# Performance work log

Hardware: AMD Instinct MI355X
Metric: run time of the kernel (lower is better)

## Reference

```python
import jax, jax.numpy as jnp
import numpy as np

EMBED = 512
NHEAD = 16
HDIM = EMBED // NHEAD
HIDDEN = 512  # Mlp hidden is hard-coded to 512
EPS_LN = 1e-6
EPS_ATT = 1e-6


def layernorm(x, gamma, beta):
    mu = jnp.mean(x, axis=-1, keepdims=True)
    var = jnp.mean(jnp.square(x - mu), axis=-1, keepdims=True)
    return (x - mu) * jax.lax.rsqrt(var + EPS_LN) * gamma + beta


def setup_inputs() -> dict:
    key = jax.random.key(0)
    ks = jax.random.split(key, 16)
    B, N, C = 8, 4096, EMBED
    s = 1.0 / np.sqrt(C)
    inp = {
        "x": jax.random.normal(ks[0], (B, N, C), dtype=jnp.float32),
        # projection weights stored as (in, out); torch Linear uses x @ W.T
        "Wq": jax.random.normal(ks[1], (C, C), dtype=jnp.float32) * s,
        "Wk": jax.random.normal(ks[2], (C, C), dtype=jnp.float32) * s,
        "Wv": jax.random.normal(ks[3], (C, C), dtype=jnp.float32) * s,
        "Wm": jax.random.normal(ks[4], (C, C), dtype=jnp.float32) * s,
        "W1": jax.random.normal(ks[5], (C, HIDDEN), dtype=jnp.float32) * s,
        "b1": jax.random.normal(ks[6], (HIDDEN,), dtype=jnp.float32) * 1e-6,
        "W2": jax.random.normal(ks[7], (HIDDEN, C), dtype=jnp.float32) * (1.0 / np.sqrt(HIDDEN)),
        "b2": jax.random.normal(ks[8], (C,), dtype=jnp.float32) * 1e-6,
        "g_att": jnp.ones((C,), dtype=jnp.float32),
        "b_att": jnp.zeros((C,), dtype=jnp.float32),
        "g_ffn": jnp.ones((C,), dtype=jnp.float32),
        "b_ffn": jnp.zeros((C,), dtype=jnp.float32),
    }
    return inp


def reference(x, Wq, Wk, Wv, Wm, W1, b1, W2, b2, g_att, b_att, g_ffn, b_ffn):
    B, N, C = x.shape
    # --- attention sub-block ---
    h = layernorm(x, g_att, b_att)
    q = (h @ Wq).reshape(B, N, NHEAD, HDIM)
    k = (h @ Wk).reshape(B, N, NHEAD, HDIM)
    v = (h @ Wv).reshape(B, N, NHEAD, HDIM)
    Q = jax.nn.elu(q) + 1.0  # feature map: elu(x)+1
    K = jax.nn.elu(k) + 1.0
    v = v / N
    KV = jnp.einsum('nshd,nshv->nhdv', K, v)
    Z = 1.0 / (jnp.einsum('nlhd,nhd->nlh', Q, K.sum(axis=1)) + EPS_ATT)
    msg = jnp.einsum('nlhd,nhdv->nlhv', Q, KV) * Z[..., None] * N
    msg = msg.reshape(B, N, C) @ Wm
    x = x + msg
    # --- feed-forward sub-block ---
    h2 = layernorm(x, g_ffn, b_ffn)
    f = jax.nn.gelu(h2 @ W1 + b1, approximate=False) @ W2 + b2
    return x + f
```

## Files before the change

kernel.cpp:

```cpp
#include <hip/hip_runtime.h>
#include <hip/hip_bf16.h>
#include <math.h>

typedef unsigned short u16;
typedef __attribute__((ext_vector_type(8))) __bf16 bf16x8;
typedef __attribute__((ext_vector_type(4))) float floatx4;

#define SEQ   4096
#define BATCH 8
#define ROWS  32768
#define C     512
#define NH    16
#define HD    32

__device__ inline u16 f2bf(float f) {
    union { float f; unsigned u; } v; v.f = f;
    unsigned r = (v.u + 0x7FFFu + ((v.u >> 16) & 1u)) >> 16;
    return (u16)r;
}
__device__ inline float bf2f(u16 h) {
    union { unsigned u; float f; } v; v.u = ((unsigned)h) << 16;
    return v.f;
}

__device__ inline void g2lds16(const u16* g, u16* l) {
    __builtin_amdgcn_global_load_lds((const __attribute__((address_space(1))) unsigned*)g,
                                     (__attribute__((address_space(3))) unsigned*)l, 16, 0, 0);
}

__global__ __launch_bounds__(256) void prep_weights(
    const float* __restrict__ Wq, const float* __restrict__ Wk,
    const float* __restrict__ Wv, const float* __restrict__ Wm,
    const float* __restrict__ W1, const float* __restrict__ W2,
    u16* __restrict__ Wqkvt, u16* __restrict__ Wmt,
    u16* __restrict__ W1t, u16* __restrict__ W2t)
{
    int blk = blockIdx.x;
    int mat = blk >> 6;
    int tile = blk & 63;
    int k0 = (tile >> 3) * 64, n0 = (tile & 7) * 64;
    const float* src; u16* dst;
    switch (mat) {
        case 0: src = Wq; dst = Wqkvt;              break;
        case 1: src = Wk; dst = Wqkvt + 512*512;    break;
        case 2: src = Wv; dst = Wqkvt + 2*512*512;  break;
        case 3: src = Wm; dst = Wmt;                break;
        case 4: src = W1; dst = W1t;                break;
        default: src = W2; dst = W2t;               break;
    }
    __shared__ float ts[64][65];
    int t = threadIdx.x;
    #pragma unroll
    for (int i = 0; i < 16; i++) {
        int e = i * 256 + t;
        int kr = e >> 6, nc = e & 63;
        ts[kr][nc] = src[(size_t)(k0 + kr) * 512 + n0 + nc];
    }
    __syncthreads();
    #pragma unroll
    for (int i = 0; i < 2; i++) {
        int e = i * 256 + t;
        int nr = e >> 3, kc0 = (e & 7) * 8;
        union { uint4 v; u16 u[8]; } o;
        #pragma unroll
        for (int q = 0; q < 8; q++) o.u[q] = f2bf(ts[kc0 + q][nr]);
        *(uint4*)(dst + (size_t)(n0 + nr) * 512 + k0 + kc0) = o.v;
    }
}

__global__ __launch_bounds__(256) void ln_kernel(
    const float* __restrict__ in, const float* __restrict__ g,
    const float* __restrict__ b, u16* __restrict__ out)
{
    int row  = blockIdx.x * 4 + (threadIdx.x >> 6);
    int lane = threadIdx.x & 63;
    const float* p = in + (size_t)row * C + lane * 8;
    float4 v0 = *(const float4*)p;
    float4 v1 = *(const float4*)(p + 4);
    float s  = v0.x + v0.y + v0.z + v0.w + v1.x + v1.y + v1.z + v1.w;
    float s2 = v0.x*v0.x + v0.y*v0.y + v0.z*v0.z + v0.w*v0.w
             + v1.x*v1.x + v1.y*v1.y + v1.z*v1.z + v1.w*v1.w;
    #pragma unroll
    for (int off = 1; off < 64; off <<= 1) {
        s  += __shfl_xor(s, off);
        s2 += __shfl_xor(s2, off);
    }
    float mean = s * (1.f / C);
    float var  = s2 * (1.f / C) - mean * mean;
    float inv  = rsqrtf(var + 1e-6f);
    int c = lane * 8;
    float4 g0 = *(const float4*)(g + c), g1 = *(const float4*)(g + c + 4);
    float4 b0 = *(const float4*)(b + c), b1 = *(const float4*)(b + c + 4);
    union { uint4 v; u16 u[8]; } o;
    o.u[0] = f2bf((v0.x - mean) * inv * g0.x + b0.x);
    o.u[1] = f2bf((v0.y - mean) * inv * g0.y + b0.y);
    o.u[2] = f2bf((v0.z - mean) * inv * g0.z + b0.z);
    o.u[3] = f2bf((v0.w - mean) * inv * g0.w + b0.w);
    o.u[4] = f2bf((v1.x - mean) * inv * g1.x + b1.x);
    o.u[5] = f2bf((v1.y - mean) * inv * g1.y + b1.y);
    o.u[6] = f2bf((v1.z - mean) * inv * g1.z + b1.z);
    o.u[7] = f2bf((v1.w - mean) * inv * g1.w + b1.w);
    *(uint4*)(out + (size_t)row * C + c) = o.v;
}

template <int EPI>
__global__ __launch_bounds__(256, 2) void gemm_tile(
    const u16* __restrict__ A, const u16* __restrict__ Bt,
    int K, int ldc, int nx, int ypx,
    u16* __restrict__ outb, float* __restrict__ outf,
    const float* __restrict__ bias, const float* __restrict__ resid)
{
    __shared__ u16 lsA[128 * 64];
    __shared__ u16 lsB[128 * 64];
    const int t = threadIdx.x;
    const int w = t >> 6, l = t & 63, lr = l & 15, quad = l >> 4;
    const int g = blockIdx.x;
    const int xcd = g & 7;
    const int q = g >> 3;
    const int npg = nx * 2;
    const int grp = q / npg, rem = q - grp * npg;
    const int tx = rem >> 1;
    const int ty = xcd * ypx + grp * 2 + (rem & 1);
    const int m0 = ty * 128, n0 = tx * 128;
    const int RW = (w >> 1) * 64, CW = (w & 1) * 64;

    floatx4 acc[4][4];
    #pragma unroll
    for (int i = 0; i < 4; i++)
        #pragma unroll
        for (int j = 0; j < 4; j++) { floatx4 z = {0.f, 0.f, 0.f, 0.f}; acc[i][j] = z; }

    const int srow = w * 32 + (l >> 3);
    const int scol = (((l & 7) - (l >> 3)) & 7) * 8;
    const u16* Ag = A  + (size_t)(m0 + srow) * K + scol;
    const u16* Bg = Bt + (size_t)(n0 + srow) * K + scol;
    u16* lAw = lsA + w * 2048;
    u16* lBw = lsB + w * 2048;

    for (int kk = 0; kk < K; kk += 64) {
        __syncthreads();
        #pragma unroll
        for (int c = 0; c < 4; c++) {
            g2lds16(Ag + (size_t)(c * 8) * K + kk, lAw + c * 512);
            g2lds16(Bg + (size_t)(c * 8) * K + kk, lBw + c * 512);
        }
        __syncthreads();
        #pragma unroll
        for (int ks = 0; ks < 2; ks++) {
            bf16x8 af[4], bfr[4];
            const int m = ((ks * 4 + quad + (lr & 7)) & 7) * 8;
            #pragma unroll
            for (int i = 0; i < 4; i++) {
                af[i]  = *(const bf16x8*)(lsA + (RW + i * 16 + lr) * 64 + m);
                bfr[i] = *(const bf16x8*)(lsB + (CW + i * 16 + lr) * 64 + m);
            }
            #pragma unroll
            for (int i = 0; i < 4; i++)
                #pragma unroll
                for (int j = 0; j < 4; j++)
                    acc[i][j] = __builtin_amdgcn_mfma_f32_16x16x32_bf16(af[i], bfr[j], acc[i][j], 0, 0, 0);
        }
    }

    #pragma unroll
    for (int i = 0; i < 4; i++) {
        #pragma unroll
        for (int j = 0; j < 4; j++) {
            #pragma unroll
            for (int r = 0; r < 4; r++) {
                int row = m0 + RW + i * 16 + quad * 4 + r;
                int col = n0 + CW + j * 16 + lr;
                float v = acc[i][j][r];
                size_t idx = (size_t)row * ldc + col;
                if constexpr (EPI == 0) {
                    if (col < 1024) v = v > 0.f ? v + 1.f : __expf(v);
                    else            v *= (1.0f / SEQ);
                    outb[idx] = f2bf(v);
                } else if constexpr (EPI == 1) {
                    outf[idx] = resid[idx] + v;
                } else if constexpr (EPI == 2) {
                    v += bias[col];
                    v = 0.5f * v * (1.f + erff(v * 0.70710678118f));
                    outb[idx] = f2bf(v);
                } else {
                    outf[idx] = outf[idx] + v + bias[col];
                }
            }
        }
    }
}

__global__ __launch_bounds__(256) void kv_reduce(
    const u16* __restrict__ qkv, float* __restrict__ Pkv, float* __restrict__ PKsum)
{
    const int bh = blockIdx.x;
    const int b = bh >> 4, h = bh & 15;
    const int chunk = blockIdx.y;
    const int t = threadIdx.x;
    const int w = t >> 6, l = t & 63, lr = l & 15, quad = l >> 4;
    __shared__ u16 lds[4 * 2 * 2048];

    const int sbase = chunk * 512 + w * 128;
    const u16* qbase = qkv + (size_t)b * SEQ * 1536 + 512 + h * HD;

    const int sl0 = l >> 2;
    const int sl1 = 16 + sl0;
    const int cl  = l & 3;
    const int cg0 = (cl + (sl0 >> 3)) & 3;
    const int cg1 = (cl + (sl1 >> 3)) & 3;
    const int gof0 = sl0 * 1536 + cg0 * 8;
    const int gof1 = sl1 * 1536 + cg1 * 8;

    u16* myl = lds + w * 4096;

    const int offA0 = quad * 256 + ((((lr >> 3) + 0) - quad) & 3) * 8 + (lr & 7);
    const int offA1 = quad * 256 + ((((lr >> 3) + 2) - quad) & 3) * 8 + (lr & 7);

    floatx4 a00 = {0,0,0,0}, a01 = {0,0,0,0}, a10 = {0,0,0,0}, a11 = {0,0,0,0};
    float ks0 = 0.f, ks1 = 0.f;

    {
        const u16* gK = qbase + (size_t)sbase * 1536;
        g2lds16(gK + gof0,       myl);
        g2lds16(gK + gof1,       myl + 512);
        g2lds16(gK + 512 + gof0, myl + 1024);
        g2lds16(gK + 512 + gof1, myl + 1536);
    }
    #pragma unroll
    for (int st = 0; st < 4; st++) {
        if (st < 3) {
            const u16* gK = qbase + (size_t)(sbase + (st + 1) * 32) * 1536;
            u16* nl = myl + ((st + 1) & 1) * 2048;
            g2lds16(gK + gof0,       nl);
            g2lds16(gK + gof1,       nl + 512);
            g2lds16(gK + 512 + gof0, nl + 1024);
            g2lds16(gK + 512 + gof1, nl + 1536);
        }
        __syncthreads();
        const u16* lK = myl + (st & 1) * 2048;
        const u16* lV = lK + 1024;
        union { bf16x8 v; u16 u[8]; } fa0, fa1, fb0, fb1;
        #pragma unroll
        for (int j = 0; j < 8; j++) {
            fa0.u[j] = lK[offA0 + j * 32];
            fa1.u[j] = lK[offA1 + j * 32];
            fb0.u[j] = lV[offA0 + j * 32];
            fb1.u[j] = lV[offA1 + j * 32];
        }
        #pragma unroll
        for (int j = 0; j < 8; j++) { ks0 += bf2f(fa0.u[j]); ks1 += bf2f(fa1.u[j]); }
        a00 = __builtin_amdgcn_mfma_f32_16x16x32_bf16(fa0.v, fb0.v, a00, 0, 0, 0);
        a01 = __builtin_amdgcn_mfma_f32_16x16x32_bf16(fa0.v, fb1.v, a01, 0, 0, 0);
        a10 = __builtin_amdgcn_mfma_f32_16x16x32_bf16(fa1.v, fb0.v, a10, 0, 0, 0);
        a11 = __builtin_amdgcn_mfma_f32_16x16x32_bf16(fa1.v, fb1.v, a11, 0, 0, 0);
    }

    const int p = bh * 32 + chunk * 4 + w;
    float* dst = Pkv + (size_t)p * 1024;
    floatx4 accs[2][2] = {{a00, a01}, {a10, a11}};
    #pragma unroll
    for (int i = 0; i < 2; i++)
        #pragma unroll
        for (int j = 0; j < 2; j++)
            #pragma unroll
            for (int r = 0; r < 4; r++)
                dst[(i * 16 + quad * 4 + r) * 32 + j * 16 + lr] = accs[i][j][r];

    float k0 = ks0 + __shfl_xor(ks0, 16); k0 += __shfl_xor(k0, 32);
    float k1 = ks1 + __shfl_xor(ks1, 16); k1 += __shfl_xor(k1, 32);
    if (quad == 0) {
        PKsum[p * 32 + lr]      = k0;
        PKsum[p * 32 + 16 + lr] = k1;
    }
}

__global__ __launch_bounds__(256) void kv_final(
    const float* __restrict__ Pkv, const float* __restrict__ PKsum,
    float* __restrict__ KV, float* __restrict__ Ksum)
{
    const int blk = blockIdx.x;
    const int bh = blk >> 2, part = blk & 3;
    const int t = threadIdx.x;
    const float* src = Pkv + (size_t)bh * 32 * 1024 + part * 256 + t;
    float a = 0.f;
    #pragma unroll 4
    for (int p = 0; p < 32; p++) a += src[(size_t)p * 1024];
    KV[(size_t)bh * 1024 + part * 256 + t] = a;
    if (part == 0 && t < 32) {
        float s = 0.f;
        for (int p = 0; p < 32; p++) s += PKsum[(bh * 32 + p) * 32 + t];
        Ksum[bh * 32 + t] = s;
    }
}

__global__ __launch_bounds__(256) void msg_kernel(
    const u16* __restrict__ qkv, const float* __restrict__ KV,
    const float* __restrict__ Ksum, u16* __restrict__ msg)
{
    int blk = blockIdx.x;
    int b = blk >> 7;
    int r0 = (blk & 127) * 32;
    int t = threadIdx.x;
    int h = t >> 4;
    int vd = (t & 15) * 2;
    float kv0[32], kv1[32], ksr[32];
    const float* kvh = KV + ((size_t)b * 16 + h) * 1024;
    const float* ksh = Ksum + (b * 16 + h) * 32;
    #pragma unroll
    for (int d = 0; d < 32; d++) {
        kv0[d] = kvh[d * 32 + vd];
        kv1[d] = kvh[d * 32 + vd + 1];
        ksr[d] = ksh[d];
    }
    __shared__ u16 Qs[4 * 512];
    const int srr = t >> 6;
    const int scc = (t & 63) * 8;
    for (int rg = 0; rg < 32; rg += 4) {
        size_t row = (size_t)b * SEQ + r0 + rg;
        uint4 qv = *(const uint4*)(qkv + (row + srr) * 1536 + scc);
        __syncthreads();
        *(uint4*)(Qs + srr * 512 + scc) = qv;
        __syncthreads();
        #pragma unroll
        for (int r2 = 0; r2 < 4; r2++) {
            const u16* qp = Qs + r2 * 512 + h * HD;
            float q[32];
            #pragma unroll
            for (int i0 = 0; i0 < 32; i0 += 8) {
                union { uint4 v; u16 u[8]; } uu;
                uu.v = *(const uint4*)(qp + i0);
                #pragma unroll
                for (int jq = 0; jq < 8; jq++) q[i0 + jq] = bf2f(uu.u[jq]);
            }
            float zdot = 0.f, m0 = 0.f, m1 = 0.f;
            #pragma unroll
            for (int d = 0; d < 32; d++) {
                float qd = q[d];
                zdot += qd * ksr[d];
                m0   += qd * kv0[d];
                m1   += qd * kv1[d];
            }
            float z = (float)SEQ / (zdot + 1e-6f);
            unsigned pack = (unsigned)f2bf(m0 * z) | ((unsigned)f2bf(m1 * z) << 16);
            *(unsigned*)(msg + (row + r2) * C + h * HD + vd) = pack;
        }
    }
}

extern "C" void kernel_launch(void* const* d_in, const int* in_sizes, int n_in,
                              void* d_out, int out_size, void* d_ws, size_t ws_size,
                              hipStream_t stream) {
    const float* x     = (const float*)d_in[0];
    const float* Wq    = (const float*)d_in[1];
    const float* Wk    = (const float*)d_in[2];
    const float* Wv    = (const float*)d_in[3];
    const float* Wm    = (const float*)d_in[4];
    const float* W1    = (const float*)d_in[5];
    const float* b1    = (const float*)d_in[6];
    const float* W2    = (const float*)d_in[7];
    const float* b2    = (const float*)d_in[8];
    const float* g_att = (const float*)d_in[9];
    const float* b_att = (const float*)d_in[10];
    const float* g_ffn = (const float*)d_in[11];
    const float* b_ffn = (const float*)d_in[12];
    float* out = (float*)d_out;

    char* ws = (char*)d_ws;
    u16*   Wqkvt = (u16*)(ws);
    u16*   Wmt   = (u16*)(ws + 0x180000);
    u16*   W1t   = (u16*)(ws + 0x200000);
    u16*   W2t   = (u16*)(ws + 0x280000);
    float* KV    = (float*)(ws + 0x300000);
    float* Ksum  = (float*)(ws + 0x380000);
    u16*   hb    = (u16*)(ws + 0x400000);
    float* Pkv   = (float*)(ws + 0x400000);
    float* PKsum = (float*)(ws + 0x1400000);
    u16*   qkv   = (u16*)(ws + 0x2400000);
    u16*   h2    = qkv;
    u16*   f1    = (u16*)(ws + 0x4400000);

    prep_weights<<<6 * 64, 256, 0, stream>>>(Wq, Wk, Wv, Wm, W1, W2,
                                             Wqkvt, Wmt, W1t, W2t);
    ln_kernel<<<ROWS / 4, 256, 0, stream>>>(x, g_att, b_att, hb);
    gemm_tile<0><<<3072, 256, 0, stream>>>(hb, Wqkvt, 512, 1536, 12, 32,
                                           qkv, nullptr, nullptr, nullptr);
    kv_reduce<<<dim3(128, 8), 256, 0, stream>>>(qkv, Pkv, PKsum);
    kv_final<<<512, 256, 0, stream>>>(Pkv, PKsum, KV, Ksum);
    msg_kernel<<<1024, 256, 0, stream>>>(qkv, KV, Ksum, hb);
    gemm_tile<1><<<1024, 256, 0, stream>>>(hb, Wmt, 512, 512, 4, 32,
                                           nullptr, out, nullptr, x);
    ln_kernel<<<ROWS / 4, 256, 0, stream>>>(out, g_ffn, b_ffn, h2);
    gemm_tile<2><<<1024, 256, 0, stream>>>(h2, W1t, 512, 512, 4, 32,
                                           f1, nullptr, b1, nullptr);
    gemm_tile<3><<<1024, 256, 0, stream>>>(f1, W2t, 512, 512, 4, 32,
                                           nullptr, out, b2, nullptr);
}
```

Before: 383.1 us.

## Fuse Wm projection GEMM with residual add and FFN layernorm

Adds a GEMM kernel whose blocks cover full 512-column rows (64 rows by 512 cols per block), so the residual add and the second layernorm can run in the epilogue. Row statistics are reduced across lanes and waves through shared memory. This removes the separate ln_kernel launch and its re-read of the fp32 residual output. The cost is a large LDS footprint (about 72KB), fewer blocks (512) and a different tile shape, which may lower occupancy. Variance is computed as E[x^2]-mean^2, which is less numerically stable.

Measured after the change: 432.4 us. 12.9% more time.

```diff
diff --git a/kernel.cpp b/kernel.cpp
--- a/kernel.cpp
+++ b/kernel.cpp
@@ -190,6 +190,134 @@
     }
 }
 
+__global__ __launch_bounds__(512, 4) void gemm_wmln(
+    const u16* __restrict__ A, const u16* __restrict__ Bt,
+    const float* __restrict__ resid, const float* __restrict__ gf,
+    const float* __restrict__ bf, float* __restrict__ out,
+    u16* __restrict__ h2)
+{
+    __shared__ u16 lsA[64 * 64];
+    __shared__ u16 lsB[512 * 64];
+    __shared__ float ps[64][4][2];
+    __shared__ float stats[64][2];
+
+    const int t = threadIdx.x;
+    const int w = t >> 6, l = t & 63, lr = l & 15, quad = l >> 4;
+    const int wr = w >> 2, wc = w & 3;
+    const int m0 = blockIdx.x * 64;
+
+    const int srow = l >> 3;
+    const int scol = (((l & 7) - srow) & 7) * 8;
+    const u16* Ag = A  + (size_t)(m0 + w * 8 + srow) * 512 + scol;
+    const u16* Bg = Bt + (size_t)(w * 64 + srow) * 512 + scol;
+    u16* lAw = lsA + w * 512;
+    u16* lBw = lsB + w * 4096;
+
+    floatx4 acc[2][8];
+    #pragma unroll
+    for (int i = 0; i < 2; i++)
+        #pragma unroll
+        for (int j = 0; j < 8; j++) { floatx4 z = {0.f, 0.f, 0.f, 0.f}; acc[i][j] = z; }
+
+    for (int kk = 0; kk < 512; kk += 64) {
+        __syncthreads();
+        g2lds16(Ag + kk, lAw);
+        #pragma unroll
+        for (int c = 0; c < 8; c++)
+            g2lds16(Bg + (size_t)(c * 8) * 512 + kk, lBw + c * 512);
+        __syncthreads();
+        #pragma unroll
+        for (int ks = 0; ks < 2; ks++) {
+            bf16x8 af[2], bfr[8];
+            const int m = ((ks * 4 + quad + (lr & 7)) & 7) * 8;
+            af[0] = *(const bf16x8*)(lsA + (wr * 32 + lr) * 64 + m);
+            af[1] = *(const bf16x8*)(lsA + (wr * 32 + 16 + lr) * 64 + m);
+            #pragma unroll
+            for (int j = 0; j < 8; j++)
+                bfr[j] = *(const bf16x8*)(lsB + (wc * 128 + j * 16 + lr) * 64 + m);
+            #pragma unroll
+            for (int i = 0; i < 2; i++)
+                #pragma unroll
+                for (int j = 0; j < 8; j++)
+                    acc[i][j] = __builtin_amdgcn_mfma_f32_16x16x32_bf16(af[i], bfr[j], acc[i][j], 0, 0, 0);
+        }
+    }
+
+    float s[2][4], s2[2][4];
+    #pragma unroll
+    for (int i = 0; i < 2; i++)
+        #pragma unroll
+        for (int r = 0; r < 4; r++) { s[i][r] = 0.f; s2[i][r] = 0.f; }
+    #pragma unroll
+    for (int i = 0; i < 2; i++) {
+        #pragma unroll
+        for (int j = 0; j < 8; j++) {
+            #pragma unroll
+            for (int r = 0; r < 4; r++) {
+                int row = m0 + wr * 32 + i * 16 + quad * 4 + r;
+                int col = wc * 128 + j * 16 + lr;
+                size_t idx = (size_t)row * 512 + col;
+                float x2 = resid[idx] + acc[i][j][r];
+                out[idx] = x2;
+                acc[i][j][r] = x2;
+                s[i][r]  += x2;
+                s2[i][r] += x2 * x2;
+            }
+        }
+    }
+    #pragma unroll
+    for (int i = 0; i < 2; i++)
+        #pragma unroll
+        for (int r = 0; r < 4; r++) {
+            #pragma unroll
+            for (int off = 1; off < 16; off <<= 1) {
+                s[i][r]  += __shfl_xor(s[i][r], off);
+                s2[i][r] += __shfl_xor(s2[i][r], off);
+            }
+        }
+    if (lr == 0) {
+        #pragma unroll
+        for (int i = 0; i < 2; i++)
+            #pragma unroll
+            for (int r = 0; r < 4; r++) {
+                int rl = wr * 32 + i * 16 + quad * 4 + r;
+                ps[rl][wc][0] = s[i][r];
+                ps[rl][wc][1] = s2[i][r];
+            }
+    }
+    __syncthreads();
+    if (t < 64) {
+        float ssum = ps[t][0][0] + ps[t][1][0] + ps[t][2][0] + ps[t][3][0];
+        float ssq  = ps[t][0][1] + ps[t][1][1] + ps[t][2][1] + ps[t][3][1];
+        float mean = ssum * (1.f / C);
+        float var  = ssq * (1.f / C) - mean * mean;
+        stats[t][0] = mean;
+        stats[t][1] = rsqrtf(var + 1e-6f);
+    }
+    __syncthreads();
+    float gv[8], bv[8];
+    #pragma unroll
+    for (int j = 0; j < 8; j++) {
+        int col = wc * 128 + j * 16 + lr;
+        gv[j] = gf[col];
+        bv[j] = bf[col];
+    }
+    #pragma unroll
+    for (int i = 0; i < 2; i++) {
+        #pragma unroll
+        for (int r = 0; r < 4; r++) {
+            int rl = wr * 32 + i * 16 + quad * 4 + r;
+            float mean = stats[rl][0], inv = stats[rl][1];
+            #pragma unroll
+            for (int j = 0; j < 8; j++) {
+                int col = wc * 128 + j * 16 + lr;
+                float h = (acc[i][j][r] - mean) * inv * gv[j] + bv[j];
+                h2[(size_t)(m0 + rl) * 512 + col] = f2bf(h);
+            }
+        }
+    }
+}
+
 __global__ __launch_bounds__(256) void kv_reduce(
     const u16* __restrict__ qkv, float* __restrict__ Pkv, float* __restrict__ PKsum)
 {
@@ -387,9 +515,7 @@
     kv_reduce<<<dim3(128, 8), 256, 0, stream>>>(qkv, Pkv, PKsum);
     kv_final<<<512, 256, 0, stream>>>(Pkv, PKsum, KV, Ksum);
     msg_kernel<<<1024, 256, 0, stream>>>(qkv, KV, Ksum, hb);
-    gemm_tile<1><<<1024, 256, 0, stream>>>(hb, Wmt, 512, 512, 4, 32,
-                                           nullptr, out, nullptr, x);
-    ln_kernel<<<ROWS / 4, 256, 0, stream>>>(out, g_ffn, b_ffn, h2);
+    gemm_wmln<<<512, 512, 0, stream>>>(hb, Wmt, x, g_ffn, b_ffn, out, h2);
     gemm_tile<2><<<1024, 256, 0, stream>>>(h2, W1t, 512, 512, 4, 32,
                                            f1, nullptr, b1, nullptr);
     gemm_tile<3><<<1024, 256, 0, stream>>>(f1, W2t, 512, 512, 4, 32,
```
